# Performance work log

Hardware: AMD Instinct MI355X
Metric: run time of the kernel (lower is better)

The kernel has to match this reference:

```python
import jax, jax.numpy as jnp
import numpy as np

NUM_TOKENS = 8192
TOKEN_DIM = 256
N = 65536
TOPK = 5
DECAY = 0.1      # cur_decay (set_decay_updates never called -> stays at init decay)
EPS = 1e-5
TEMP = 1.0


def setup_inputs() -> dict:
    key = jax.random.key(0)
    k1, k2 = jax.random.split(key)
    return {
        "inputs_flatten": jax.random.normal(k1, (N, TOKEN_DIM), dtype=jnp.float32),
        "embed": jax.random.normal(k2, (NUM_TOKENS, TOKEN_DIM), dtype=jnp.float32),
        "cluster_size": jnp.zeros((NUM_TOKENS,), dtype=jnp.float32),
        "cluster_sum": jnp.zeros((NUM_TOKENS,), dtype=jnp.float32),
        "embed_avg": jnp.zeros((NUM_TOKENS, TOKEN_DIM), dtype=jnp.float32),
    }


def reference(inputs_flatten, embed, cluster_size, cluster_sum, embed_avg):
    x = inputs_flatten                              # [N, D]
    # squared euclidean distances to codebook: [N, K]
    distances = (jnp.sum(x * x, axis=1, keepdims=True)
                 + jnp.sum(embed * embed, axis=1)
                 - 2.0 * (x @ embed.T))
    # top-k nearest codes (smallest distance)
    neg_topk, topk_idx = jax.lax.top_k(-distances, TOPK)   # [N, k]
    topk_dist = -neg_topk
    weights = jax.nn.softmax(-topk_dist / TEMP, axis=1)    # [N, k]
    # scatter soft weights into dense one-hot-ish encodings [N, K]
    rows = jnp.arange(x.shape[0])[:, None]
    encodings = jnp.zeros_like(distances).at[rows, topk_idx].set(weights)
    encoding_indices = jnp.argmax(encodings, axis=1)[:, None]   # [N, 1]

    # training-mode EMA codebook update (module default is training=True)
    encoding_sum = jnp.sum(encodings, axis=0)                   # [K]
    new_cluster_sum = cluster_sum + encoding_sum
    new_cluster_size = cluster_size * DECAY + encoding_sum * (1.0 - DECAY)
    embed_sum = encodings.T @ x                                 # [K, D]
    new_embed_avg = embed_avg * DECAY + embed_sum * (1.0 - DECAY)
    smoothed = (new_cluster_size + EPS) / (jnp.sum(new_cluster_size) + NUM_TOKENS * EPS)
    cs = smoothed * jnp.sum(new_cluster_size)
    new_embed = new_embed_avg / cs[:, None]                     # embed.data.copy_(...)

    quantize = encodings @ new_embed                            # [N, D]
    quantize = jax.lax.stop_gradient(quantize - x) + x          # straight-through
    return quantize, encoding_indices
```

## Files before the change

### kernel.cpp

```cpp
#include <hip/hip_runtime.h>
#include <hip/hip_bf16.h>
#include <math.h>
#include <limits.h>

#define NROWS 65536
#define DIM   256
#define NCODE 8192
#define NTOPK 5

typedef __attribute__((ext_vector_type(4))) float     f32x4;
typedef __attribute__((ext_vector_type(4))) int       i32x4;

#define WS_ESWZ   0u
#define WS_CINIT  2097152u
#define WS_XQ     2129920u
#define WS_NEWEMB 2129920u
#define WS_ENTR   10518528u
#define WS_IDX5   18907136u
#define WS_W5     20217856u
#define WS_ENCSUM 21528576u
#define WS_CNT    21561344u
#define WS_OFFS   21594112u
#define WS_CURS   21626880u
#define WS_SFAC   21659648u

#define ENT_PER_BLK 64
#define NENT (NROWS * NTOPK)

__device__ __forceinline__ void gl_lds16(const void* g, void* l) {
  __builtin_amdgcn_global_load_lds(
      (const __attribute__((address_space(1))) unsigned int*)g,
      (__attribute__((address_space(3))) unsigned int*)l, 16, 0, 0);
}

__device__ __forceinline__ unsigned f2key(float f) {
  unsigned u = __float_as_uint(f);
  return (u & 0x80000000u) ? ~u : (u | 0x80000000u);
}
__device__ __forceinline__ float key2f(unsigned k) {
  unsigned u = (k & 0x80000000u) ? (k ^ 0x80000000u) : ~k;
  return __uint_as_float(u);
}

__device__ __forceinline__ int pk4(f32x4 v) {
  int r = 0;
  #pragma unroll
  for (int j = 0; j < 4; ++j) {
    float q = fminf(127.f, fmaxf(-127.f, rintf(16.f * v[j])));
    r |= ((int)q & 255) << (8 * j);
  }
  return r;
}

__global__ __launch_bounds__(256) void k_prepall(const float* __restrict__ embed,
                                                 const float* __restrict__ x,
                                                 signed char* __restrict__ eswz,
                                                 int* __restrict__ cinit,
                                                 signed char* __restrict__ xq) {
  if (blockIdx.x < NCODE) {
    const int code = blockIdx.x;
    const int d = threadIdx.x;
    float v = embed[code * DIM + d];
    float qf = fminf(127.f, fmaxf(-127.f, rintf(16.f * v)));
    int q = (int)qf;
    __shared__ unsigned char rb[256];
    __shared__ int red[4];
    rb[d] = (unsigned char)(q & 255);
    int e2 = q * q;
    #pragma unroll
    for (int off = 32; off; off >>= 1) e2 += __shfl_down(e2, off);
    const int lane = d & 63, w = d >> 6;
    if (lane == 0) red[w] = e2;
    __syncthreads();
    if (d == 0) {
      int s = red[0] + red[1] + red[2] + red[3];
      cinit[code] = -(s >> 1) * 8192 + code;
    }
    if (d < 64) {
      unsigned u = (unsigned)rb[4 * d] | ((unsigned)rb[4 * d + 1] << 8) |
                   ((unsigned)rb[4 * d + 2] << 16) | ((unsigned)rb[4 * d + 3] << 24);
      const int cs = (d >> 2) ^ (code & 15);
      ((unsigned*)(eswz + code * 256))[(cs << 2) | (d & 3)] = u;
    }
  } else {
    const int t = threadIdx.x;
    const int s = t >> 6, q = (t >> 4) & 3, ln = t & 15;
    const unsigned row0 = (blockIdx.x - NCODE) * 64;
    #pragma unroll
    for (int g = 0; g < 4; ++g) {
      const unsigned row = row0 + g * 16 + ln;
      const float* xr = x + row * DIM + s * 64 + q * 16;
      i32x4 dw;
      #pragma unroll
      for (int d = 0; d < 4; ++d) dw[d] = pk4(*(const f32x4*)(xr + d * 4));
      *(i32x4*)(xq + (unsigned)(row0 + g * 16) * 256u + (unsigned)t * 16u) = dw;
    }
  }
}


struct PList { int a, b, c, d; };

__device__ __forceinline__ void ladder(PList& P, int t) {
  int c0 = min(P.a, t); P.a = max(P.a, t);
  int c1 = min(P.b, c0); P.b = max(P.b, c0);
  int c2 = min(P.c, c1); P.c = max(P.c, c1);
  P.d = max(P.d, c2);
}

__device__ __forceinline__ void psel(PList& P, i32x4 acc, i32x4 en) {
  int p0 = acc[0] * 8192 + en[0];
  int p1 = acc[1] * 8192 + en[1];
  int p2 = acc[2] * 8192 + en[2];
  int p3 = acc[3] * 8192 + en[3];
  int h1 = max(p0, p1);
  int h2 = max(p2, p3);
  int t1 = max(h1, h2);
  if (__any(t1 > P.d)) {
    int l1 = min(p0, p1), l2 = min(p2, p3);
    int t2 = max(min(h1, h2), max(l1, l2));
    ladder(P, t1);
    if (__any(t2 > P.d)) ladder(P, t2);
  }
}

#define GBODY(IT, SL, NS)                                                      \
  {                                                                            \
    const int tg = ((IT) + 2 < 64) ? (IT) + 2 : 63;                            \
    const signed char* src = esw_h + (unsigned)tg * 8192u;                     \
    gl_lds16(src + tid * 16, &ebuf[NS][tid * 16]);                             \
    gl_lds16(src + 4096 + tid * 16, &ebuf[NS][4096 + tid * 16]);               \
    i32x4 enC0 = *(const i32x4*)(cin_h + tg * 32 + q * 4);                     \
    i32x4 enC1 = *(const i32x4*)(cin_h + tg * 32 + 16 + q * 4);                \
    asm volatile("s_waitcnt vmcnt(8)\n\ts_barrier" ::: "memory");              \
    const signed char* eb = ebuf[SL];                                          \
    i32x4 a00 = {0, 0, 0, 0}, a01 = a00, a10 = a00, a11 = a00;                 \
    __builtin_amdgcn_s_setprio(1);                                             \
    _Pragma("unroll")                                                          \
    for (int s = 0; s < 4; ++s) {                                              \
      const int chunk = (4 * s + q) ^ ln;                                      \
      i32x4 ea0 = *(const i32x4*)&eb[ln * 256 + chunk * 16];                   \
      i32x4 ea1 = *(const i32x4*)&eb[4096 + ln * 256 + chunk * 16];            \
      a00 = __builtin_amdgcn_mfma_i32_16x16x64_i8(ea0, xf[0][s], a00, 0, 0, 0);\
      a10 = __builtin_amdgcn_mfma_i32_16x16x64_i8(ea0, xf[1][s], a10, 0, 0, 0);\
      a01 = __builtin_amdgcn_mfma_i32_16x16x64_i8(ea1, xf[0][s], a01, 0, 0, 0);\
      a11 = __builtin_amdgcn_mfma_i32_16x16x64_i8(ea1, xf[1][s], a11, 0, 0, 0);\
    }                                                                          \
    __builtin_amdgcn_s_setprio(0);                                             \
    psel(P0, a00, enA0); psel(P0, a01, enA1);                                  \
    psel(P1, a10, enA0); psel(P1, a11, enA1);                                  \
    enA0 = enB0; enA1 = enB1; enB0 = enC0; enB1 = enC1;                        \
  }

__global__ __launch_bounds__(256, 4) void k_gemm(const signed char* __restrict__ xq,
                                                 const signed char* __restrict__ eswz,
                                                 const int* __restrict__ cinit,
                                                 int* __restrict__ candk) {
  __shared__ signed char ebuf[4][8192];
  const int tid = threadIdx.x;
  const int lane = tid & 63, wave = tid >> 6;
  const int q = lane >> 4, ln = lane & 15;
  const int quarter = blockIdx.x & 3, rblk = blockIdx.x >> 2;
  const int wrow0 = rblk * 128 + wave * 32;
  const signed char* esw_h = eswz + (unsigned)quarter * (2048u * 256u);
  const int* cin_h = cinit + quarter * 2048;

  gl_lds16(esw_h + tid * 16, &ebuf[0][tid * 16]);
  gl_lds16(esw_h + 4096 + tid * 16, &ebuf[0][4096 + tid * 16]);
  gl_lds16(esw_h + 8192 + tid * 16, &ebuf[1][tid * 16]);
  gl_lds16(esw_h + 8192 + 4096 + tid * 16, &ebuf[1][4096 + tid * 16]);
  i32x4 enA0 = *(const i32x4*)(cin_h + q * 4);
  i32x4 enA1 = *(const i32x4*)(cin_h + 16 + q * 4);
  i32x4 enB0 = *(const i32x4*)(cin_h + 32 + q * 4);
  i32x4 enB1 = *(const i32x4*)(cin_h + 48 + q * 4);

  i32x4 xf[2][4];
  {
    const signed char* xb = xq + (unsigned)wrow0 * 256u;
    #pragma unroll
    for (int t = 0; t < 2; ++t)
      #pragma unroll
      for (int s = 0; s < 4; ++s)
        xf[t][s] = *(const i32x4*)(xb + t * 4096 + s * 1024 + lane * 16);
  }

  PList P0 = {INT_MIN, INT_MIN, INT_MIN, INT_MIN};
  PList P1 = P0;

  #pragma unroll 1
  for (int ob = 0; ob < 16; ++ob) {
    const int it0 = ob * 4;
    GBODY(it0 + 0, 0, 2)
    GBODY(it0 + 1, 1, 3)
    GBODY(it0 + 2, 2, 0)
    GBODY(it0 + 3, 3, 1)
  }

  {
    const int row0 = wrow0 + ln;
    i32x4 pk0 = {P0.a, P0.b, P0.c, P0.d};
    *(i32x4*)&candk[row0 * 64 + quarter * 16 + q * 4] = pk0;
    const int row1 = wrow0 + 16 + ln;
    i32x4 pk1 = {P1.a, P1.b, P1.c, P1.d};
    *(i32x4*)&candk[row1 * 64 + quarter * 16 + q * 4] = pk1;
  }
}

__global__ __launch_bounds__(256) void k_refine(const float* __restrict__ x,
                                                const float* __restrict__ embed,
                                                const int* __restrict__ candk,
                                                float* __restrict__ out_idx,
                                                int* __restrict__ idx5,
                                                float* __restrict__ w5,
                                                float* __restrict__ enc_sum,
                                                unsigned* __restrict__ cnt) {
  __shared__ float sh[4][8][66];
  const int wave = threadIdx.x >> 6, l = threadIdx.x & 63;
  const int row = blockIdx.x * 4 + wave;

  int k = candk[row * 64 + l];
  int cd[8];
  #pragma unroll
  for (int j = 0; j < 8; ++j) {
    int m = k;
    #pragma unroll
    for (int off = 1; off < 64; off <<= 1) m = max(m, __shfl_xor(m, off));
    cd[j] = m & 8191;
    if (k == m) k = INT_MIN;
  }

  const float* xr = x + (unsigned)row * DIM;
  const f32x4 xv = *(const f32x4*)(xr + 4 * l);
  const float t0 = -2.f * xv[0], t1 = -2.f * xv[1];
  const float t2 = -2.f * xv[2], t3 = -2.f * xv[3];

  #pragma unroll
  for (int ci = 0; ci < 8; ++ci) {
    const f32x4 e = *(const f32x4*)(embed + (unsigned)cd[ci] * DIM + 4 * l);
    float p = e[0] * (e[0] + t0);
    p = fmaf(e[1], e[1] + t1, p);
    p = fmaf(e[2], e[2] + t2, p);
    p = fmaf(e[3], e[3] + t3, p);
    sh[wave][ci][l] = p;
  }
  asm volatile("s_waitcnt lgkmcnt(0)" ::: "memory");

  const int c = l >> 3, sub = l & 7;
  const float* sp = &sh[wave][c][sub * 8];
  f32x4 v0 = *(const f32x4*)sp;
  f32x4 v1 = *(const f32x4*)(sp + 4);
  double s64 = (double)v0[0] + (double)v0[1] + (double)v0[2] + (double)v0[3]
             + (double)v1[0] + (double)v1[1] + (double)v1[2] + (double)v1[3];
  s64 += __shfl_xor(s64, 1);
  s64 += __shfl_xor(s64, 2);
  s64 += __shfl_xor(s64, 4);

  double sc = __shfl(s64, (l & 7) * 8);
  unsigned fkey = f2key((float)sc);
  const int myc = cd[l & 7];

  bool used = false;
  int codes[5]; float svals[5];
  #pragma unroll
  for (int j = 0; j < 5; ++j) {
    unsigned kk = used ? 0xFFFFFFFFu : fkey;
    unsigned mm = kk;
    #pragma unroll
    for (int off = 1; off < 8; off <<= 1) mm = min(mm, (unsigned)__shfl_xor((int)mm, off));
    int cc = (kk == mm) ? myc : 0x7FFFFFFF;
    #pragma unroll
    for (int off = 1; off < 8; off <<= 1) cc = min(cc, __shfl_xor(cc, off));
    used = used || (myc == cc);
    codes[j] = cc;
    svals[j] = key2f(mm);
  }

  float ex[5], sum = 0.f;
  #pragma unroll
  for (int j = 0; j < 5; ++j) { ex[j] = expf(-(svals[j] - svals[0])); sum += ex[j]; }
  const float inv = 1.f / sum;

  if (l == 0) {
    out_idx[row] = (float)codes[0];
    #pragma unroll
    for (int j = 0; j < 5; ++j) {
      float w = ex[j] * inv;
      idx5[row * 5 + j] = codes[j];
      w5[row * 5 + j] = w;
      atomicAdd(&enc_sum[codes[j]], w);
      atomicAdd(&cnt[codes[j]], 1u);
    }
  }
}

__global__ __launch_bounds__(256) void k_scan(const unsigned* __restrict__ cnt,
                                              unsigned* __restrict__ offs,
                                              unsigned* __restrict__ cursor,
                                              const float* __restrict__ enc_sum,
                                              const float* __restrict__ cluster_size,
                                              float* __restrict__ sfac) {
  __shared__ unsigned part[256];
  __shared__ double sred[256];
  const int t = threadIdx.x;
  unsigned s = 0;
  for (int i = 0; i < 32; ++i) s += cnt[t * 32 + i];
  part[t] = s;
  double ds = 0.0;
  for (int i = t; i < NCODE; i += 256)
    ds += 0.1 * (double)cluster_size[i] + 0.9 * (double)enc_sum[i];
  sred[t] = ds;
  __syncthreads();
  #pragma unroll
  for (int off = 1; off < 256; off <<= 1) {
    unsigned v = (t >= off) ? part[t - off] : 0u;
    __syncthreads();
    part[t] += v;
    __syncthreads();
  }
  #pragma unroll
  for (int off = 128; off; off >>= 1) {
    if (t < off) sred[t] += sred[t + off];
    __syncthreads();
  }
  if (t == 0) {
    double S = sred[0];
    sfac[0] = (float)(S / (S + (double)NCODE * 1e-5));
  }
  unsigned off0 = part[t] - s;
  for (int i = 0; i < 32; ++i) {
    unsigned c = cnt[t * 32 + i];
    offs[t * 32 + i] = off0;
    cursor[t * 32 + i] = off0;
    off0 += c;
  }
}

__global__ __launch_bounds__(256) void k_fill(const int* __restrict__ idx5,
                                              const float* __restrict__ w5,
                                              unsigned* __restrict__ cursor,
                                              uint2* __restrict__ entries) {
  const int i = blockIdx.x * 256 + threadIdx.x;
  if (i >= NENT) return;
  const unsigned c = (unsigned)idx5[i];
  const float w = w5[i];
  const unsigned row = (unsigned)i / 5u;
  const unsigned slot = atomicAdd(&cursor[c], 1u);
  entries[slot] = make_uint2((c << 16) | row, __float_as_uint(w));
}

__global__ __launch_bounds__(256) void k_accum2(const float* __restrict__ x,
                                                const uint2* __restrict__ entries,
                                                float* __restrict__ embsum) {
  __shared__ uint2 ent[ENT_PER_BLK];
  const int t = threadIdx.x;
  const unsigned base = blockIdx.x * ENT_PER_BLK;
  if (t < ENT_PER_BLK * 2)
    ((unsigned*)ent)[t] = ((const unsigned*)(entries + base))[t];
  __syncthreads();

  float acc = 0.f;
  unsigned cur = ent[0].x >> 16;
  #pragma unroll 8
  for (int i = 0; i < ENT_PER_BLK; ++i) {
    const uint2 e = ent[i];
    const unsigned code = e.x >> 16;
    const unsigned row = e.x & 0xFFFFu;
    const float w = __uint_as_float(e.y);
    if (code != cur) {
      atomicAdd(&embsum[cur * DIM + t], acc);
      acc = 0.f; cur = code;
    }
    acc = fmaf(w, x[row * DIM + t], acc);
  }
  atomicAdd(&embsum[cur * DIM + t], acc);
}

__global__ __launch_bounds__(256) void k_norm(const float* __restrict__ embed_avg,
                                              const float* __restrict__ cluster_size,
                                              const float* __restrict__ enc_sum,
                                              const float* __restrict__ sfac,
                                              float* __restrict__ embsum ) {
  const int k = blockIdx.x, d = threadIdx.x;
  const float ncs = 0.1f * cluster_size[k] + 0.9f * enc_sum[k];
  const float cs = (ncs + 1e-5f) * sfac[0];
  const unsigned o = (unsigned)k * DIM + d;
  embsum[o] = (0.1f * embed_avg[o] + 0.9f * embsum[o]) / cs;
}

__global__ __launch_bounds__(256) void k_quant(const int* __restrict__ idx5,
                                               const float* __restrict__ w5,
                                               const float* __restrict__ newemb,
                                               float* __restrict__ out) {
  const int l = threadIdx.x & 63, wv = threadIdx.x >> 6;
  const int rb = blockIdx.x * 16;
  #pragma unroll
  for (int r = 0; r < 4; ++r) {
    const int row = rb + wv * 4 + r;
    f32x4 acc = {0.f, 0.f, 0.f, 0.f};
    #pragma unroll
    for (int j = 0; j < 5; ++j) {
      const int c = idx5[row * 5 + j];
      const float wg = w5[row * 5 + j];
      const f32x4 e = *(const f32x4*)(newemb + (unsigned)c * DIM + 4 * l);
      acc[0] = fmaf(wg, e[0], acc[0]);
      acc[1] = fmaf(wg, e[1], acc[1]);
      acc[2] = fmaf(wg, e[2], acc[2]);
      acc[3] = fmaf(wg, e[3], acc[3]);
    }
    *(f32x4*)(out + (unsigned)row * DIM + 4 * l) = acc;
  }
}

extern "C" void kernel_launch(void* const* d_in, const int* in_sizes, int n_in,
                              void* d_out, int out_size, void* d_ws, size_t ws_size,
                              hipStream_t stream) {
  const float* x            = (const float*)d_in[0];
  const float* embed        = (const float*)d_in[1];
  const float* cluster_size = (const float*)d_in[2];
  const float* embed_avg    = (const float*)d_in[4];

  char* w = (char*)d_ws;
  signed char*    eswz   = (signed char*)(w + WS_ESWZ);
  int*            cinit  = (int*)(w + WS_CINIT);
  signed char*    xq     = (signed char*)(w + WS_XQ);
  int*            idx5   = (int*)(w + WS_IDX5);
  float*          w5     = (float*)(w + WS_W5);
  float*          encsum = (float*)(w + WS_ENCSUM);
  unsigned*       cnt    = (unsigned*)(w + WS_CNT);
  unsigned*       offs   = (unsigned*)(w + WS_OFFS);
  unsigned*       curs   = (unsigned*)(w + WS_CURS);
  float*          sfac   = (float*)(w + WS_SFAC);
  float*          embsum = (float*)(w + WS_NEWEMB);
  uint2*          entr   = (uint2*)(w + WS_ENTR);

  float* out_q   = (float*)d_out;
  float* out_idx = out_q + (size_t)NROWS * DIM;
  int*   candk   = (int*)d_out;

  hipMemsetAsync(w + WS_ENCSUM, 0, 65536, stream);

  k_prepall<<<NCODE + NROWS / 64, 256, 0, stream>>>(embed, x, eswz, cinit, xq);
  k_gemm<<<NROWS / 128 * 4, 256, 0, stream>>>(xq, eswz, cinit, candk);
  hipMemsetAsync(w + WS_NEWEMB, 0, (size_t)NCODE * DIM * 4, stream);
  k_refine<<<NROWS / 4, 256, 0, stream>>>(x, embed, candk, out_idx, idx5, w5, encsum, cnt);
  k_scan<<<1, 256, 0, stream>>>(cnt, offs, curs, encsum, cluster_size, sfac);
  k_fill<<<(NENT + 255) / 256, 256, 0, stream>>>(idx5, w5, curs, entr);
  k_accum2<<<NENT / ENT_PER_BLK, 256, 0, stream>>>(x, entr, embsum);
  k_norm<<<NCODE, 256, 0, stream>>>(embed_avg, cluster_size, encsum, sfac, embsum);
  k_quant<<<NROWS / 16, 256, 0, stream>>>(idx5, w5, embsum, out_q);
}
```

Before: 425.4 us.

## Fuse codebook normalization into quantize and make accum wave-per-segment with float4

Removes the separate k_norm kernel by computing the EMA-blended, normalized codebook row on the fly inside k_quant, so each referenced code row is renormalized per use. k_accum2 now gives each wave its own entry segment and has each lane handle four dims with float4 loads, instead of one 256-thread block per segment with a shared-memory staging step. This drops a full pass over the 8 MB codebook and one launch. In exchange, k_quant reads two codebook arrays per candidate plus per-code scalars and does a divide, and accum issues four scalar atomics per lane flush.

```diff
diff --git a/kernel.cpp b/kernel.cpp
--- a/kernel.cpp
+++ b/kernel.cpp
@@ -351,48 +351,52 @@
 __global__ __launch_bounds__(256) void k_accum2(const float* __restrict__ x,
                                                 const uint2* __restrict__ entries,
                                                 float* __restrict__ embsum) {
-  __shared__ uint2 ent[ENT_PER_BLK];
-  const int t = threadIdx.x;
-  const unsigned base = blockIdx.x * ENT_PER_BLK;
-  if (t < ENT_PER_BLK * 2)
-    ((unsigned*)ent)[t] = ((const unsigned*)(entries + base))[t];
-  __syncthreads();
-
-  float acc = 0.f;
-  unsigned cur = ent[0].x >> 16;
+  const int l = threadIdx.x & 63;
+  const int wv = __builtin_amdgcn_readfirstlane(threadIdx.x >> 6);
+  const unsigned seg = blockIdx.x * 4u + (unsigned)wv;
+  const uint2* ep = entries + seg * ENT_PER_BLK;
+
+  f32x4 acc = {0.f, 0.f, 0.f, 0.f};
+  unsigned cur = ep[0].x >> 16;
   #pragma unroll 8
   for (int i = 0; i < ENT_PER_BLK; ++i) {
-    const uint2 e = ent[i];
+    const uint2 e = ep[i];
     const unsigned code = e.x >> 16;
     const unsigned row = e.x & 0xFFFFu;
     const float w = __uint_as_float(e.y);
     if (code != cur) {
-      atomicAdd(&embsum[cur * DIM + t], acc);
-      acc = 0.f; cur = code;
-    }
-    acc = fmaf(w, x[row * DIM + t], acc);
-  }
-  atomicAdd(&embsum[cur * DIM + t], acc);
-}
-
-__global__ __launch_bounds__(256) void k_norm(const float* __restrict__ embed_avg,
-                                              const float* __restrict__ cluster_size,
-                                              const float* __restrict__ enc_sum,
-                                              const float* __restrict__ sfac,
-                                              float* __restrict__ embsum ) {
-  const int k = blockIdx.x, d = threadIdx.x;
-  const float ncs = 0.1f * cluster_size[k] + 0.9f * enc_sum[k];
-  const float cs = (ncs + 1e-5f) * sfac[0];
-  const unsigned o = (unsigned)k * DIM + d;
-  embsum[o] = (0.1f * embed_avg[o] + 0.9f * embsum[o]) / cs;
+      float* dst = embsum + cur * DIM + 4 * l;
+      atomicAdd(dst + 0, acc[0]);
+      atomicAdd(dst + 1, acc[1]);
+      atomicAdd(dst + 2, acc[2]);
+      atomicAdd(dst + 3, acc[3]);
+      acc[0] = acc[1] = acc[2] = acc[3] = 0.f;
+      cur = code;
+    }
+    const f32x4 xv = *(const f32x4*)(x + row * DIM + 4 * l);
+    acc[0] = fmaf(w, xv[0], acc[0]);
+    acc[1] = fmaf(w, xv[1], acc[1]);
+    acc[2] = fmaf(w, xv[2], acc[2]);
+    acc[3] = fmaf(w, xv[3], acc[3]);
+  }
+  float* dst = embsum + cur * DIM + 4 * l;
+  atomicAdd(dst + 0, acc[0]);
+  atomicAdd(dst + 1, acc[1]);
+  atomicAdd(dst + 2, acc[2]);
+  atomicAdd(dst + 3, acc[3]);
 }
 
 __global__ __launch_bounds__(256) void k_quant(const int* __restrict__ idx5,
                                                const float* __restrict__ w5,
-                                               const float* __restrict__ newemb,
+                                               const float* __restrict__ embsum,
+                                               const float* __restrict__ embed_avg,
+                                               const float* __restrict__ cluster_size,
+                                               const float* __restrict__ enc_sum,
+                                               const float* __restrict__ sfac,
                                                float* __restrict__ out) {
   const int l = threadIdx.x & 63, wv = threadIdx.x >> 6;
   const int rb = blockIdx.x * 16;
+  const float sf = sfac[0];
   #pragma unroll
   for (int r = 0; r < 4; ++r) {
     const int row = rb + wv * 4 + r;
@@ -401,11 +405,14 @@
     for (int j = 0; j < 5; ++j) {
       const int c = idx5[row * 5 + j];
       const float wg = w5[row * 5 + j];
-      const f32x4 e = *(const f32x4*)(newemb + (unsigned)c * DIM + 4 * l);
-      acc[0] = fmaf(wg, e[0], acc[0]);
-      acc[1] = fmaf(wg, e[1], acc[1]);
-      acc[2] = fmaf(wg, e[2], acc[2]);
-      acc[3] = fmaf(wg, e[3], acc[3]);
+      const float ncs = 0.1f * cluster_size[c] + 0.9f * enc_sum[c];
+      const float inv = wg / ((ncs + 1e-5f) * sf);
+      const f32x4 es = *(const f32x4*)(embsum + (unsigned)c * DIM + 4 * l);
+      const f32x4 ea = *(const f32x4*)(embed_avg + (unsigned)c * DIM + 4 * l);
+      acc[0] = fmaf(inv, fmaf(0.9f, es[0], 0.1f * ea[0]), acc[0]);
+      acc[1] = fmaf(inv, fmaf(0.9f, es[1], 0.1f * ea[1]), acc[1]);
+      acc[2] = fmaf(inv, fmaf(0.9f, es[2], 0.1f * ea[2]), acc[2]);
+      acc[3] = fmaf(inv, fmaf(0.9f, es[3], 0.1f * ea[3]), acc[3]);
     }
     *(f32x4*)(out + (unsigned)row * DIM + 4 * l) = acc;
   }
@@ -445,7 +452,7 @@
   k_refine<<<NROWS / 4, 256, 0, stream>>>(x, embed, candk, out_idx, idx5, w5, encsum, cnt);
   k_scan<<<1, 256, 0, stream>>>(cnt, offs, curs, encsum, cluster_size, sfac);
   k_fill<<<(NENT + 255) / 256, 256, 0, stream>>>(idx5, w5, curs, entr);
-  k_accum2<<<NENT / ENT_PER_BLK, 256, 0, stream>>>(x, entr, embsum);
-  k_norm<<<NCODE, 256, 0, stream>>>(embed_avg, cluster_size, encsum, sfac, embsum);
-  k_quant<<<NROWS / 16, 256, 0, stream>>>(idx5, w5, embsum, out_q);
-}
+  k_accum2<<<NENT / ENT_PER_BLK / 4, 256, 0, stream>>>(x, entr, embsum);
+  k_quant<<<NROWS / 16, 256, 0, stream>>>(idx5, w5, embsum, embed_avg,
+                                          cluster_size, encsum, sfac, out_q);
+}
```

New measurement: 444.9 us. +4.6%, slower.
